# Optimization experiments

Measured on AMD Instinct MI355X. Metric: run time of the kernel, lower is better.

## Reference

```python
import jax, jax.numpy as jnp
import numpy as np

DIM = 512
HEADS = 8
HEAD_DIM = DIM // HEADS
MLP_HIDDEN = int(DIM * 4.0)
B, N = 4, 2048
LS_INIT = 1e-5
EPS = 1e-5


def _layernorm(x, w, b):
    mu = jnp.mean(x, axis=-1, keepdims=True)
    var = jnp.mean(jnp.square(x - mu), axis=-1, keepdims=True)
    return (x - mu) * jax.lax.rsqrt(var + EPS) * w + b


def setup_inputs() -> dict:
    key = jax.random.key(0)
    ks = jax.random.split(key, 12)
    s = 0.02
    return {
        "x": jax.random.normal(ks[0], (B, N, DIM), jnp.float32),
        "rel_pos_bias": jax.random.normal(ks[1], (HEADS, N, N), jnp.float32),
        "qkv_w": jax.random.normal(ks[2], (DIM, 3 * DIM), jnp.float32) * s,
        "qkv_b": jnp.zeros((3 * DIM,), jnp.float32),
        "out_w": jax.random.normal(ks[3], (DIM, DIM), jnp.float32) * s,
        "out_b": jnp.zeros((DIM,), jnp.float32),
        "ln1_w": jnp.ones((DIM,), jnp.float32),
        "ln1_b": jnp.zeros((DIM,), jnp.float32),
        "ln2_w": jnp.ones((DIM,), jnp.float32),
        "ln2_b": jnp.zeros((DIM,), jnp.float32),
        "ffn_w1": jax.random.normal(ks[4], (DIM, MLP_HIDDEN), jnp.float32) * s,
        "ffn_b1": jnp.zeros((MLP_HIDDEN,), jnp.float32),
        "ffn_w2": jax.random.normal(ks[5], (MLP_HIDDEN, DIM), jnp.float32) * s,
        "ffn_b2": jnp.zeros((DIM,), jnp.float32),
        "gamma1": jnp.full((DIM,), LS_INIT, jnp.float32),
        "gamma2": jnp.full((DIM,), LS_INIT, jnp.float32),
    }


def reference(x, rel_pos_bias, qkv_w, qkv_b, out_w, out_b, ln1_w, ln1_b,
              ln2_w, ln2_b, ffn_w1, ffn_b1, ffn_w2, ffn_b2, gamma1, gamma2):
    # Pre-norm MHA with relative-position bias
    y = _layernorm(x, ln1_w, ln1_b)                       # [B,N,C]
    qkv = y @ qkv_w + qkv_b                               # [B,N,3C]
    qkv = qkv.reshape(B, N, 3, HEADS, HEAD_DIM)
    q = jnp.transpose(qkv[:, :, 0], (0, 2, 1, 3))         # [B,H,N,D]
    k = jnp.transpose(qkv[:, :, 1], (0, 2, 1, 3))
    v = jnp.transpose(qkv[:, :, 2], (0, 2, 1, 3))
    scale = 1.0 / np.sqrt(HEAD_DIM).astype(np.float32)
    attn = jnp.einsum("bhid,bhjd->bhij", q, k) * scale    # [B,H,N,N]
    attn = attn + rel_pos_bias[None]
    attn = jax.nn.softmax(attn, axis=-1)
    out = jnp.einsum("bhij,bhjd->bhid", attn, v)          # [B,H,N,D]
    out = jnp.transpose(out, (0, 2, 1, 3)).reshape(B, N, DIM)
    out = out @ out_w + out_b
    x = x + out * gamma1                                  # layer scale, no drop-path (eval)
    # FFN with exact GELU
    y2 = _layernorm(x, ln2_w, ln2_b)
    h = jax.nn.gelu(y2 @ ffn_w1 + ffn_b1, approximate=False)
    ffn_out = h @ ffn_w2 + ffn_b2
    x = x + ffn_out * gamma2
    return x
```

## Files before the change

### kernel.cpp

```cpp
#include <hip/hip_runtime.h>
#include <hip/hip_bf16.h>
#include <math.h>

#define SEQ 2048
#define BATCH 4
#define DM 512
#define NH 8
#define HD 64
#define HID 2048
#define ROWS (BATCH * SEQ)

typedef __attribute__((ext_vector_type(8))) short short8;
typedef __attribute__((ext_vector_type(4))) float f32x4;

__device__ __forceinline__ short f2bf(float f) {
    unsigned u = __float_as_uint(f);
    u += 0x7fff + ((u >> 16) & 1);
    return (short)(u >> 16);
}

__device__ __forceinline__ void gl2lds16(const void* g, void* l) {
    __builtin_amdgcn_global_load_lds(
        (const __attribute__((address_space(1))) void*)g,
        (__attribute__((address_space(3))) void*)l, 16, 0, 0);
}

__global__ __launch_bounds__(256) void tcast_all(
    const float* __restrict__ qkv_w, const float* __restrict__ out_w,
    const float* __restrict__ w1, const float* __restrict__ w2,
    short* __restrict__ o_qkv, short* __restrict__ o_out,
    short* __restrict__ o_w1, short* __restrict__ o_w2) {
    __shared__ float tile[32][33];
    int id = blockIdx.x;
    const float* W; short* O; int K, N;
    if (id < 768)       { W = qkv_w; O = o_qkv; K = 512;  N = 1536; }
    else if (id < 1024) { W = out_w; O = o_out; K = 512;  N = 512;  id -= 768; }
    else if (id < 2048) { W = w1;    O = o_w1;  K = 512;  N = 2048; id -= 1024; }
    else                { W = w2;    O = o_w2;  K = 2048; N = 512;  id -= 2048; }
    int tn = N / 32;
    int n0 = (id % tn) * 32, k0 = (id / tn) * 32;
    int tx = threadIdx.x, ty = threadIdx.y;
#pragma unroll
    for (int i = 0; i < 4; ++i)
        tile[ty + i * 8][tx] = W[(size_t)(k0 + ty + i * 8) * N + n0 + tx];
    __syncthreads();
#pragma unroll
    for (int i = 0; i < 4; ++i)
        O[(size_t)(n0 + ty + i * 8) * K + k0 + tx] = f2bf(tile[tx][ty + i * 8]);
}

__global__ __launch_bounds__(256) void ln_k(const float* __restrict__ X,
                                            const float* __restrict__ g,
                                            const float* __restrict__ bta,
                                            short* __restrict__ Y) {
    int t = threadIdx.x;
    int wv = t >> 6, ln = t & 63;
    size_t row = (size_t)blockIdx.x * 4 + wv;
    const float* xr = X + row * DM;
    float4 v0 = *(const float4*)(xr + ln * 4);
    float4 v1 = *(const float4*)(xr + 256 + ln * 4);
    float s = v0.x + v0.y + v0.z + v0.w + v1.x + v1.y + v1.z + v1.w;
    float q = v0.x * v0.x + v0.y * v0.y + v0.z * v0.z + v0.w * v0.w +
              v1.x * v1.x + v1.y * v1.y + v1.z * v1.z + v1.w * v1.w;
#pragma unroll
    for (int off = 1; off < 64; off <<= 1) {
        s += __shfl_xor(s, off);
        q += __shfl_xor(q, off);
    }
    float mean = s * (1.0f / 512.0f);
    float var = q * (1.0f / 512.0f) - mean * mean;
    float rstd = rsqrtf(var + 1e-5f);
    int c0 = ln * 4, c1 = 256 + ln * 4;
    ushort4 o0, o1;
    o0.x = (unsigned short)f2bf((v0.x - mean) * rstd * g[c0 + 0] + bta[c0 + 0]);
    o0.y = (unsigned short)f2bf((v0.y - mean) * rstd * g[c0 + 1] + bta[c0 + 1]);
    o0.z = (unsigned short)f2bf((v0.z - mean) * rstd * g[c0 + 2] + bta[c0 + 2]);
    o0.w = (unsigned short)f2bf((v0.w - mean) * rstd * g[c0 + 3] + bta[c0 + 3]);
    o1.x = (unsigned short)f2bf((v1.x - mean) * rstd * g[c1 + 0] + bta[c1 + 0]);
    o1.y = (unsigned short)f2bf((v1.y - mean) * rstd * g[c1 + 1] + bta[c1 + 1]);
    o1.z = (unsigned short)f2bf((v1.z - mean) * rstd * g[c1 + 2] + bta[c1 + 2]);
    o1.w = (unsigned short)f2bf((v1.w - mean) * rstd * g[c1 + 3] + bta[c1 + 3]);
    *(ushort4*)((unsigned short*)Y + row * DM + c0) = o0;
    *(ushort4*)((unsigned short*)Y + row * DM + c1) = o1;
}

template <int EPI, int TN>
__global__ __launch_bounds__(256) void gemm_bt(const short* __restrict__ A,
                                               const short* __restrict__ Bt,
                                               const float* __restrict__ bias,
                                               const float* __restrict__ gamma,
                                               const float* __restrict__ res,
                                               void* __restrict__ Cout,
                                               short* __restrict__ Cout2,
                                               int M, int N, int K) {
    constexpr int NI = TN / 32;
    __shared__ __attribute__((aligned(16))) short As0[128][32];
    __shared__ __attribute__((aligned(16))) short As1[128][32];
    __shared__ __attribute__((aligned(16))) short Bs0[TN][32];
    __shared__ __attribute__((aligned(16))) short Bs1[TN][32];
    int t = threadIdx.x;
    int w = t >> 6, ln = t & 63;
    int quad = ln >> 4, l15 = ln & 15;
    int n0 = blockIdx.x * TN, m0 = blockIdx.y * 128;
    int wm = (w & 1) * 64, wn = (w >> 1) * (TN / 2);

    int srow0 = w * 32 + (ln >> 2);
    int srow1 = srow0 + 16;
    int srowB = w * 16 + (ln >> 2);
    int schunk = (ln & 3) * 8;
    const short* Ag0 = A + (size_t)(m0 + srow0) * K + schunk;
    const short* Ag1 = A + (size_t)(m0 + srow1) * K + schunk;
    const short* Bg0 = Bt + (size_t)(n0 + srow0) * K + schunk;
    const short* Bg1 = Bt + (size_t)(n0 + srow1) * K + schunk;
    const short* BgB = Bt + (size_t)(n0 + srowB) * K + schunk;

    f32x4 acc[4][NI];
#pragma unroll
    for (int i = 0; i < 4; ++i)
#pragma unroll
        for (int j = 0; j < NI; ++j) acc[i][j] = (f32x4){0.f, 0.f, 0.f, 0.f};

    for (int k0 = 0; k0 < K; k0 += 64) {
        __syncthreads();
        gl2lds16(Ag0 + k0, &As0[srow0][schunk]);
        gl2lds16(Ag1 + k0, &As0[srow1][schunk]);
        gl2lds16(Ag0 + k0 + 32, &As1[srow0][schunk]);
        gl2lds16(Ag1 + k0 + 32, &As1[srow1][schunk]);
        if (TN == 128) {
            gl2lds16(Bg0 + k0, &Bs0[srow0 & (TN - 1)][schunk]);
            gl2lds16(Bg1 + k0, &Bs0[srow1 & (TN - 1)][schunk]);
            gl2lds16(Bg0 + k0 + 32, &Bs1[srow0 & (TN - 1)][schunk]);
            gl2lds16(Bg1 + k0 + 32, &Bs1[srow1 & (TN - 1)][schunk]);
        } else {
            gl2lds16(BgB + k0, &Bs0[srowB & (TN - 1)][schunk]);
            gl2lds16(BgB + k0 + 32, &Bs1[srowB & (TN - 1)][schunk]);
        }
        __syncthreads();
        {
            short8 af[4], bf[NI];
#pragma unroll
            for (int mi = 0; mi < 4; ++mi)
                af[mi] = *(const short8*)&As0[wm + mi * 16 + l15][quad * 8];
#pragma unroll
            for (int ni = 0; ni < NI; ++ni)
                bf[ni] = *(const short8*)&Bs0[wn + ni * 16 + l15][quad * 8];
#pragma unroll
            for (int mi = 0; mi < 4; ++mi)
#pragma unroll
                for (int ni = 0; ni < NI; ++ni)
                    acc[mi][ni] = __builtin_amdgcn_mfma_f32_16x16x32_bf16(
                        af[mi], bf[ni], acc[mi][ni], 0, 0, 0);
        }
        {
            short8 af[4], bf[NI];
#pragma unroll
            for (int mi = 0; mi < 4; ++mi)
                af[mi] = *(const short8*)&As1[wm + mi * 16 + l15][quad * 8];
#pragma unroll
            for (int ni = 0; ni < NI; ++ni)
                bf[ni] = *(const short8*)&Bs1[wn + ni * 16 + l15][quad * 8];
#pragma unroll
            for (int mi = 0; mi < 4; ++mi)
#pragma unroll
                for (int ni = 0; ni < NI; ++ni)
                    acc[mi][ni] = __builtin_amdgcn_mfma_f32_16x16x32_bf16(
                        af[mi], bf[ni], acc[mi][ni], 0, 0, 0);
        }
    }

    if (EPI == 3 && n0 >= 1024) {
#pragma unroll
        for (int mi = 0; mi < 4; ++mi) {
#pragma unroll
            for (int ni = 0; ni < NI; ++ni) {
                int col = n0 + wn + ni * 16 + l15;
                int d = col - 1024, hh = d >> 6, dd = d & 63;
                int row0 = m0 + wm + mi * 16 + quad * 4;
                int bb = row0 >> 11, key = row0 & 2047;
                float bs = bias[col];
                ushort4 pk;
                pk.x = (unsigned short)f2bf(acc[mi][ni][0] + bs);
                pk.y = (unsigned short)f2bf(acc[mi][ni][1] + bs);
                pk.z = (unsigned short)f2bf(acc[mi][ni][2] + bs);
                pk.w = (unsigned short)f2bf(acc[mi][ni][3] + bs);
                *(ushort4*)&Cout2[((size_t)(bb * 8 + hh) * 64 + dd) * 2048 + key] = pk;
            }
        }
    } else {
#pragma unroll
        for (int mi = 0; mi < 4; ++mi) {
#pragma unroll
            for (int ni = 0; ni < NI; ++ni) {
#pragma unroll
                for (int r = 0; r < 4; ++r) {
                    int row = m0 + wm + mi * 16 + quad * 4 + r;
                    int col = n0 + wn + ni * 16 + l15;
                    float v = acc[mi][ni][r] + bias[col];
                    if (EPI == 0) {
                        ((short*)Cout)[(size_t)row * N + col] = f2bf(v);
                    } else if (EPI == 1) {
                        float u = v * fmaf(v * v, 0.0713548162f, 1.59576912f);
                        float gg = v / (1.0f + __expf(-u));
                        ((short*)Cout)[(size_t)row * N + col] = f2bf(gg);
                    } else if (EPI == 2) {
                        ((float*)Cout)[(size_t)row * N + col] =
                            fmaf(v, gamma[col], res[(size_t)row * N + col]);
                    } else {
                        float sc = (n0 < 512) ? 0.18033688f : 1.0f;
                        ((short*)Cout)[(size_t)row * 1024 + col] = f2bf(v * sc);
                    }
                }
            }
        }
    }
}

__global__ __launch_bounds__(256, 3) void attn_k(const short* __restrict__ qkv,
                                                 const short* __restrict__ vT,
                                                 const float* __restrict__ bias,
                                                 float* __restrict__ O0,
                                                 float* __restrict__ O1,
                                                 float* __restrict__ lp) {
    __shared__ __attribute__((aligned(16))) short Ks[2][64 * 64];
    __shared__ __attribute__((aligned(16))) short Vs[2][64 * 64];
    __shared__ __attribute__((aligned(16))) short Ps[4][2][16 * 64];
    int t = threadIdx.x;
    int w = t >> 6, ln = t & 63, quad = ln >> 4, l15 = ln & 15;
    int idx = blockIdx.x;
    int half = idx >> 9;
    int rest = idx & 511;
    int h = rest & 7, b = (rest >> 3) & 3, qt = rest >> 5;
    int qb = qt * 128 + w * 16;
    int jt0 = half * 16;
    int j0 = jt0 * 64;
    const size_t cbase = (size_t)b * SEQ * 1024;

    const short* qrow0 = qkv + cbase + (size_t)(qb + l15) * 1024 + h * 64;
    const short* qrow1 = qrow0 + (size_t)64 * 1024;
    short8 qf[2][2];
    qf[0][0] = *(const short8*)(qrow0 + quad * 8);
    qf[0][1] = *(const short8*)(qrow0 + 32 + quad * 8);
    qf[1][0] = *(const short8*)(qrow1 + quad * 8);
    qf[1][1] = *(const short8*)(qrow1 + 32 + quad * 8);

    int kr = t >> 3, kc = t & 7;
    int sc = (kc ^ (kr & 7)) * 8;
    const short* kgS = qkv + cbase + 512 + h * 64 + sc;
    const short* vgS = vT + (size_t)(b * 8 + h) * 64 * 2048 + sc;

    const float* bq0 = bias + (size_t)h * SEQ * SEQ +
                       (size_t)(qb + l15) * SEQ + quad * 4;
    const float* bq1 = bq0 + (size_t)64 * SEQ;

    short8 ones;
#pragma unroll
    for (int i = 0; i < 8; ++i) ones[i] = (short)0x3F80;

    f32x4 o[2][4], ol[2];
#pragma unroll
    for (int qg = 0; qg < 2; ++qg) {
#pragma unroll
        for (int db = 0; db < 4; ++db) o[qg][db] = (f32x4){0.f, 0.f, 0.f, 0.f};
        ol[qg] = (f32x4){0.f, 0.f, 0.f, 0.f};
    }

    int sw7 = l15 & 7;

    gl2lds16(kgS + (size_t)(j0 + kr) * 1024,      &Ks[0][t * 8]);
    gl2lds16(kgS + (size_t)(j0 + 32 + kr) * 1024, &Ks[0][2048 + t * 8]);
    gl2lds16(vgS + (size_t)kr * 2048 + j0,        &Vs[0][t * 8]);
    gl2lds16(vgS + (size_t)(32 + kr) * 2048 + j0, &Vs[0][2048 + t * 8]);
    float4 bbc[2][4];
#pragma unroll
    for (int ni = 0; ni < 4; ++ni) {
        bbc[0][ni] = *(const float4*)(bq0 + j0 + ni * 16);
        bbc[1][ni] = *(const float4*)(bq1 + j0 + ni * 16);
    }

    int cur = 0;
    for (int jt = jt0; jt < jt0 + 16; ++jt) {
        __syncthreads();
        int j1 = (jt < jt0 + 15) ? (jt + 1) * 64 : j0;
        int nxt = cur ^ 1;
        gl2lds16(kgS + (size_t)(j1 + kr) * 1024,      &Ks[nxt][t * 8]);
        gl2lds16(kgS + (size_t)(j1 + 32 + kr) * 1024, &Ks[nxt][2048 + t * 8]);
        gl2lds16(vgS + (size_t)kr * 2048 + j1,        &Vs[nxt][t * 8]);
        gl2lds16(vgS + (size_t)(32 + kr) * 2048 + j1, &Vs[nxt][2048 + t * 8]);

        f32x4 s4[2][4];
#pragma unroll
        for (int ni = 0; ni < 4; ++ni) {
            short8 k0 = *(const short8*)&Ks[cur][(ni * 16 + l15) * 64 + ((quad ^ sw7) * 8)];
            short8 k1 = *(const short8*)&Ks[cur][(ni * 16 + l15) * 64 + (((4 + quad) ^ sw7) * 8)];
#pragma unroll
            for (int qg = 0; qg < 2; ++qg) {
                f32x4 z = (f32x4){0.f, 0.f, 0.f, 0.f};
                z = __builtin_amdgcn_mfma_f32_16x16x32_bf16(k0, qf[qg][0], z, 0, 0, 0);
                s4[qg][ni] = __builtin_amdgcn_mfma_f32_16x16x32_bf16(k1, qf[qg][1], z, 0, 0, 0);
            }
        }
#pragma unroll
        for (int qg = 0; qg < 2; ++qg) {
#pragma unroll
            for (int ni = 0; ni < 4; ++ni) {
                float4 bb = bbc[qg][ni];
                float2 plo, phi;
                plo.x = exp2f(fmaf(bb.x, 1.44269504f, s4[qg][ni][0]));
                plo.y = exp2f(fmaf(bb.y, 1.44269504f, s4[qg][ni][1]));
                phi.x = exp2f(fmaf(bb.z, 1.44269504f, s4[qg][ni][2]));
                phi.y = exp2f(fmaf(bb.w, 1.44269504f, s4[qg][ni][3]));
                bbc[qg][ni] = *(const float4*)((qg ? bq1 : bq0) + j1 + ni * 16);
                __hip_bfloat162 l2 = __float22bfloat162_rn(plo);
                __hip_bfloat162 h2 = __float22bfloat162_rn(phi);
                union { uint2 u; } pp;
                pp.u.x = *(unsigned*)&l2;
                pp.u.y = *(unsigned*)&h2;
                int c = ni * 2 + (quad >> 1);
                *(uint2*)&Ps[w][qg][l15 * 64 + ((c ^ sw7) * 8) + (quad & 1) * 4] = pp.u;
            }
        }
#pragma unroll
        for (int kk = 0; kk < 2; ++kk) {
            short8 ap0 = *(const short8*)&Ps[w][0][l15 * 64 + (((kk * 4 + quad) ^ sw7) * 8)];
            short8 ap1 = *(const short8*)&Ps[w][1][l15 * 64 + (((kk * 4 + quad) ^ sw7) * 8)];
#pragma unroll
            for (int db = 0; db < 4; ++db) {
                short8 vv = *(const short8*)&Vs[cur][(db * 16 + l15) * 64 + (((kk * 4 + quad) ^ sw7) * 8)];
                o[0][db] = __builtin_amdgcn_mfma_f32_16x16x32_bf16(ap0, vv, o[0][db], 0, 0, 0);
                o[1][db] = __builtin_amdgcn_mfma_f32_16x16x32_bf16(ap1, vv, o[1][db], 0, 0, 0);
            }
            ol[0] = __builtin_amdgcn_mfma_f32_16x16x32_bf16(ap0, ones, ol[0], 0, 0, 0);
            ol[1] = __builtin_amdgcn_mfma_f32_16x16x32_bf16(ap1, ones, ol[1], 0, 0, 0);
        }
        cur = nxt;
    }
    float* Od = half ? O1 : O0;
    float* ld = lp + half * (32 * 2048);
#pragma unroll
    for (int qg = 0; qg < 2; ++qg) {
#pragma unroll
        for (int r = 0; r < 4; ++r) {
            int qloc = qb + qg * 64 + quad * 4 + r;
            int qrow_g = b * SEQ + qloc;
#pragma unroll
            for (int db = 0; db < 4; ++db) {
                Od[(size_t)qrow_g * DM + h * 64 + db * 16 + l15] = o[qg][db][r];
            }
            if (l15 == 0)
                ld[(size_t)(b * 8 + h) * 2048 + qloc] = ol[qg][r];
        }
    }
}

__global__ __launch_bounds__(256) void comb_k(const float* __restrict__ O0,
                                              const float* __restrict__ O1,
                                              const float* __restrict__ lp,
                                              short* __restrict__ Aout) {
    int t = threadIdx.x;
    int wv = t >> 6, ln = t & 63;
    size_t row = (size_t)blockIdx.x * 4 + wv;
    int b = (int)(row >> 11), q = (int)(row & 2047);
    int h = ln >> 3;
    float la = lp[(size_t)(b * 8 + h) * 2048 + q];
    float lb = lp[32 * 2048 + (size_t)(b * 8 + h) * 2048 + q];
    float inv = 1.0f / (la + lb);
    const float* p0 = O0 + row * DM + ln * 8;
    const float* p1 = O1 + row * DM + ln * 8;
    float4 a0 = *(const float4*)p0;
    float4 a1 = *(const float4*)(p0 + 4);
    float4 c0 = *(const float4*)p1;
    float4 c1 = *(const float4*)(p1 + 4);
    short8 o;
    o[0] = f2bf((a0.x + c0.x) * inv);
    o[1] = f2bf((a0.y + c0.y) * inv);
    o[2] = f2bf((a0.z + c0.z) * inv);
    o[3] = f2bf((a0.w + c0.w) * inv);
    o[4] = f2bf((a1.x + c1.x) * inv);
    o[5] = f2bf((a1.y + c1.y) * inv);
    o[6] = f2bf((a1.z + c1.z) * inv);
    o[7] = f2bf((a1.w + c1.w) * inv);
    *(short8*)(Aout + row * DM + ln * 8) = o;
}

extern "C" void kernel_launch(void* const* d_in, const int* in_sizes, int n_in,
                              void* d_out, int out_size, void* d_ws, size_t ws_size,
                              hipStream_t stream) {
    const float* x      = (const float*)d_in[0];
    const float* bias   = (const float*)d_in[1];
    const float* qkv_w  = (const float*)d_in[2];
    const float* qkv_b  = (const float*)d_in[3];
    const float* out_w  = (const float*)d_in[4];
    const float* out_b  = (const float*)d_in[5];
    const float* ln1_w  = (const float*)d_in[6];
    const float* ln1_b  = (const float*)d_in[7];
    const float* ln2_w  = (const float*)d_in[8];
    const float* ln2_b  = (const float*)d_in[9];
    const float* ffn_w1 = (const float*)d_in[10];
    const float* ffn_b1 = (const float*)d_in[11];
    const float* ffn_w2 = (const float*)d_in[12];
    const float* ffn_b2 = (const float*)d_in[13];
    const float* gamma1 = (const float*)d_in[14];
    const float* gamma2 = (const float*)d_in[15];
    float* out = (float*)d_out;

    short* wqkvT = (short*)d_ws;
    short* woutT = wqkvT + (size_t)1536 * 512;
    short* w1T   = woutT + (size_t)512 * 512;
    short* w2T   = w1T + (size_t)2048 * 512;
    short* y1    = w2T + (size_t)512 * 2048;
    short* qkvB  = y1 + (size_t)ROWS * DM;
    short* vTb   = qkvB + (size_t)ROWS * 1024;
    short* aoutB = vTb + (size_t)32 * 64 * 2048;
    float* x1    = (float*)(aoutB + (size_t)ROWS * DM);
    float* opart1 = x1 + (size_t)ROWS * DM;
    float* lpart  = opart1 + (size_t)ROWS * DM;
    float* opart0 = x1;
    short* hB    = qkvB;

    tcast_all<<<3072, dim3(32, 8), 0, stream>>>(qkv_w, out_w, ffn_w1, ffn_w2,
                                                wqkvT, woutT, w1T, w2T);
    ln_k<<<ROWS / 4, 256, 0, stream>>>(x, ln1_w, ln1_b, y1);
    gemm_bt<3, 128><<<dim3(1536 / 128, ROWS / 128), 256, 0, stream>>>(
        y1, wqkvT, qkv_b, nullptr, nullptr, qkvB, vTb, ROWS, 1536, 512);
    attn_k<<<1024, 256, 0, stream>>>(qkvB, vTb, bias, opart0, opart1, lpart);
    comb_k<<<ROWS / 4, 256, 0, stream>>>(opart0, opart1, lpart, aoutB);
    gemm_bt<2, 64><<<dim3(512 / 64, ROWS / 128), 256, 0, stream>>>(
        aoutB, woutT, out_b, gamma1, x, x1, nullptr, ROWS, 512, 512);
    ln_k<<<ROWS / 4, 256, 0, stream>>>(x1, ln2_w, ln2_b, y1);
    gemm_bt<1, 128><<<dim3(2048 / 128, ROWS / 128), 256, 0, stream>>>(
        y1, w1T, ffn_b1, nullptr, nullptr, hB, nullptr, ROWS, 2048, 512);
    gemm_bt<2, 64><<<dim3(512 / 64, ROWS / 128), 256, 0, stream>>>(
        hB, w2T, ffn_b2, gamma2, x1, out, nullptr, ROWS, 512, 2048);
}
```

Baseline: 438.5 us.

## Precompute bias as log2e-scaled bf16 in MFMA fragment layout, seed accumulators with it

Adds a pre-pass kernel that converts the fp32 relative-position bias into bf16. The pass also pre-multiplies it by log2(e) and stores it in the per-lane MFMA accumulator layout. The attention kernel then loads half as many bias bytes per tile and uses the bias as the initial accumulator of the QK^T MFMA, which removes the per-element fma before exp2. The cost is an extra full pass over the large bias tensor on every call, plus reduced bias precision from rounding to bf16.

```diff
diff --git a/kernel.cpp b/kernel.cpp
--- a/kernel.cpp
+++ b/kernel.cpp
@@ -47,6 +47,39 @@
 #pragma unroll
     for (int i = 0; i < 4; ++i)
         O[(size_t)(n0 + ty + i * 8) * K + k0 + tx] = f2bf(tile[tx][ty + i * 8]);
+}
+
+__global__ __launch_bounds__(256) void bias_prep(const float* __restrict__ bias,
+                                                 short* __restrict__ biasP) {
+    __shared__ float tl[4][16][68];
+    int t = threadIdx.x;
+    int w = t >> 6, ln = t & 63;
+    int quad = ln >> 4, l15 = ln & 15;
+    int tau = blockIdx.x * 4 + w;
+    int jtK = tau & 31;
+    int g = (tau >> 5) & 127;
+    int h = tau >> 12;
+    const float* src = bias + (size_t)h * SEQ * SEQ + (size_t)g * 16 * SEQ + jtK * 64;
+#pragma unroll
+    for (int i = 0; i < 4; ++i) {
+        int row = i * 4 + quad;
+        int col = l15 * 4;
+        *(float4*)&tl[w][row][col] = *(const float4*)(src + (size_t)row * SEQ + col);
+    }
+    short* dst = biasP + (size_t)tau * 1024 + ln * 4;
+#pragma unroll
+    for (int ni = 0; ni < 4; ++ni) {
+        float4 v = *(const float4*)&tl[w][l15][ni * 16 + quad * 4];
+        float2 lo, hi;
+        lo.x = v.x * 1.44269504f; lo.y = v.y * 1.44269504f;
+        hi.x = v.z * 1.44269504f; hi.y = v.w * 1.44269504f;
+        __hip_bfloat162 l2 = __float22bfloat162_rn(lo);
+        __hip_bfloat162 h2 = __float22bfloat162_rn(hi);
+        uint2 pp;
+        pp.x = *(unsigned*)&l2;
+        pp.y = *(unsigned*)&h2;
+        *(uint2*)(dst + (size_t)ni * 256) = pp;
+    }
 }
 
 __global__ __launch_bounds__(256) void ln_k(const float* __restrict__ X,
@@ -217,7 +250,7 @@
 
 __global__ __launch_bounds__(256, 3) void attn_k(const short* __restrict__ qkv,
                                                  const short* __restrict__ vT,
-                                                 const float* __restrict__ bias,
+                                                 const short* __restrict__ biasP,
                                                  float* __restrict__ O0,
                                                  float* __restrict__ O1,
                                                  float* __restrict__ lp) {
@@ -248,9 +281,9 @@
     const short* kgS = qkv + cbase + 512 + h * 64 + sc;
     const short* vgS = vT + (size_t)(b * 8 + h) * 64 * 2048 + sc;
 
-    const float* bq0 = bias + (size_t)h * SEQ * SEQ +
-                       (size_t)(qb + l15) * SEQ + quad * 4;
-    const float* bq1 = bq0 + (size_t)64 * SEQ;
+    int g0 = qt * 8 + w;
+    const short* bp0 = biasP + ((size_t)(h * 128 + g0) * 32) * 1024 + ln * 4;
+    const short* bp1 = biasP + ((size_t)(h * 128 + g0 + 4) * 32) * 1024 + ln * 4;
 
     short8 ones;
 #pragma unroll
@@ -270,17 +303,18 @@
     gl2lds16(kgS + (size_t)(j0 + 32 + kr) * 1024, &Ks[0][2048 + t * 8]);
     gl2lds16(vgS + (size_t)kr * 2048 + j0,        &Vs[0][t * 8]);
     gl2lds16(vgS + (size_t)(32 + kr) * 2048 + j0, &Vs[0][2048 + t * 8]);
-    float4 bbc[2][4];
+    uint2 bbc[2][4];
 #pragma unroll
     for (int ni = 0; ni < 4; ++ni) {
-        bbc[0][ni] = *(const float4*)(bq0 + j0 + ni * 16);
-        bbc[1][ni] = *(const float4*)(bq1 + j0 + ni * 16);
+        bbc[0][ni] = *(const uint2*)(bp0 + (size_t)jt0 * 1024 + ni * 256);
+        bbc[1][ni] = *(const uint2*)(bp1 + (size_t)jt0 * 1024 + ni * 256);
     }
 
     int cur = 0;
     for (int jt = jt0; jt < jt0 + 16; ++jt) {
         __syncthreads();
-        int j1 = (jt < jt0 + 15) ? (jt + 1) * 64 : j0;
+        int jn = (jt < jt0 + 15) ? (jt + 1) : jt;
+        int j1 = jn * 64;
         int nxt = cur ^ 1;
         gl2lds16(kgS + (size_t)(j1 + kr) * 1024,      &Ks[nxt][t * 8]);
         gl2lds16(kgS + (size_t)(j1 + 32 + kr) * 1024, &Ks[nxt][2048 + t * 8]);
@@ -294,7 +328,13 @@
             short8 k1 = *(const short8*)&Ks[cur][(ni * 16 + l15) * 64 + (((4 + quad) ^ sw7) * 8)];
 #pragma unroll
             for (int qg = 0; qg < 2; ++qg) {
-                f32x4 z = (f32x4){0.f, 0.f, 0.f, 0.f};
+                uint2 bb = bbc[qg][ni];
+                f32x4 z;
+                z[0] = __uint_as_float(bb.x << 16);
+                z[1] = __uint_as_float(bb.x & 0xffff0000u);
+                z[2] = __uint_as_float(bb.y << 16);
+                z[3] = __uint_as_float(bb.y & 0xffff0000u);
+                bbc[qg][ni] = *(const uint2*)((qg ? bp1 : bp0) + (size_t)jn * 1024 + ni * 256);
                 z = __builtin_amdgcn_mfma_f32_16x16x32_bf16(k0, qf[qg][0], z, 0, 0, 0);
                 s4[qg][ni] = __builtin_amdgcn_mfma_f32_16x16x32_bf16(k1, qf[qg][1], z, 0, 0, 0);
             }
@@ -303,13 +343,11 @@
         for (int qg = 0; qg < 2; ++qg) {
 #pragma unroll
             for (int ni = 0; ni < 4; ++ni) {
-                float4 bb = bbc[qg][ni];
                 float2 plo, phi;
-                plo.x = exp2f(fmaf(bb.x, 1.44269504f, s4[qg][ni][0]));
-                plo.y = exp2f(fmaf(bb.y, 1.44269504f, s4[qg][ni][1]));
-                phi.x = exp2f(fmaf(bb.z, 1.44269504f, s4[qg][ni][2]));
-                phi.y = exp2f(fmaf(bb.w, 1.44269504f, s4[qg][ni][3]));
-                bbc[qg][ni] = *(const float4*)((qg ? bq1 : bq0) + j1 + ni * 16);
+                plo.x = exp2f(s4[qg][ni][0]);
+                plo.y = exp2f(s4[qg][ni][1]);
+                phi.x = exp2f(s4[qg][ni][2]);
+                phi.y = exp2f(s4[qg][ni][3]);
                 __hip_bfloat162 l2 = __float22bfloat162_rn(plo);
                 __hip_bfloat162 h2 = __float22bfloat162_rn(phi);
                 union { uint2 u; } pp;
@@ -414,15 +452,17 @@
     float* x1    = (float*)(aoutB + (size_t)ROWS * DM);
     float* opart1 = x1 + (size_t)ROWS * DM;
     float* lpart  = opart1 + (size_t)ROWS * DM;
+    short* biasPw = (short*)(lpart + 2 * 32 * 2048);
     float* opart0 = x1;
     short* hB    = qkvB;
 
     tcast_all<<<3072, dim3(32, 8), 0, stream>>>(qkv_w, out_w, ffn_w1, ffn_w2,
                                                 wqkvT, woutT, w1T, w2T);
+    bias_prep<<<8192, 256, 0, stream>>>(bias, biasPw);
     ln_k<<<ROWS / 4, 256, 0, stream>>>(x, ln1_w, ln1_b, y1);
     gemm_bt<3, 128><<<dim3(1536 / 128, ROWS / 128), 256, 0, stream>>>(
         y1, wqkvT, qkv_b, nullptr, nullptr, qkvB, vTb, ROWS, 1536, 512);
-    attn_k<<<1024, 256, 0, stream>>>(qkvB, vTb, bias, opart0, opart1, lpart);
+    attn_k<<<1024, 256, 0, stream>>>(qkvB, vTb, biasPw, opart0, opart1, lpart);
     comb_k<<<ROWS / 4, 256, 0, stream>>>(opart0, opart1, lpart, aoutB);
     gemm_bt<2, 64><<<dim3(512 / 64, ROWS / 128), 256, 0, stream>>>(
         aoutB, woutT, out_b, gamma1, x, x1, nullptr, ROWS, 512, 512);
```

After: 463.9 us. 1.06x slower.
